# Kernel tuning notes

Hardware: AMD Instinct MI355X
Metric: run time of the kernel (lower is better)

## Reference

```python
import jax, jax.numpy as jnp
import numpy as np

N_LEVELS = 16
N_FEAT = 2
LOG2_T = 19
T = 2 ** LOG2_T
BASE_RES = 2 ** 4
MAX_RES = 2 ** 11
PER_LEVEL_SCALE = np.exp((np.log(MAX_RES) - np.log(BASE_RES)) / (N_LEVELS - 1))
RESOLUTIONS = [int(np.floor(BASE_RES * PER_LEVEL_SCALE ** lv)) + 1 for lv in range(N_LEVELS)]
INIT_ACTIVE_LEVEL = 8
N_POINTS = 1048576
N_OUT = N_LEVELS * N_FEAT
# tcnn spatial hashing primes
P1 = jnp.uint32(2654435761)
P2 = jnp.uint32(805459861)


def _level_lookup(x, tbl, res):
    """x: [N,3] in [0,1], tbl: [T,F], res: python int grid resolution."""
    pos = x * (res - 1)                       # [N,3]
    c0 = jnp.clip(jnp.floor(pos).astype(jnp.int32), 0, res - 2)
    w = pos - c0.astype(pos.dtype)            # [N,3] trilinear fractions
    feats = jnp.zeros((x.shape[0], tbl.shape[-1]), dtype=tbl.dtype)
    dense = (res ** 3) <= T                   # static per level: dense grid vs hashed
    for dz in (0, 1):
        for dy in (0, 1):
            for dx in (0, 1):
                offs = jnp.array([dx, dy, dz], jnp.int32)
                c = c0 + offs                 # [N,3] corner int coords
                if dense:
                    idx = c[:, 0] + res * (c[:, 1] + res * c[:, 2])
                else:
                    cu = c.astype(jnp.uint32)
                    idx = ((cu[:, 0]) ^ (cu[:, 1] * P1) ^ (cu[:, 2] * P2)) & jnp.uint32(T - 1)
                    idx = idx.astype(jnp.int32)
                # trilinear corner weight: prod over axes of (w if offs==1 else 1-w)
                wc = jnp.prod(jnp.where(offs == 1, w, 1.0 - w), axis=-1)  # [N]
                feats = feats + tbl[idx] * wc[:, None]
    return feats


def setup_inputs() -> dict:
    key = jax.random.key(0)
    k1, k2 = jax.random.split(key)
    x = jax.random.uniform(k1, (N_POINTS, 3), dtype=jnp.float32)
    # tcnn-style small uniform init of the hash table
    table = jax.random.uniform(k2, (N_LEVELS, T, N_FEAT), dtype=jnp.float32,
                               minval=-1e-4, maxval=1e-4)
    mask = jnp.concatenate([
        jnp.ones(INIT_ACTIVE_LEVEL * N_FEAT, jnp.float32),
        jnp.zeros((N_LEVELS - INIT_ACTIVE_LEVEL) * N_FEAT, jnp.float32),
    ])
    return {"x": x, "table": table, "mask": mask}


def reference(x, table, mask):
    # multi-resolution hash grid encoding + progressive level mask
    outs = [_level_lookup(x, table[lv], RESOLUTIONS[lv]) for lv in range(N_LEVELS)]
    enc = jnp.concatenate(outs, axis=-1)      # [N, 32]
    return enc * mask
```

## Files before the change

### kernel.cpp

```cpp
#include <hip/hip_runtime.h>
#include <cstdint>
#include <cstddef>


namespace {

constexpr int      kNLevels = 16;
constexpr uint32_t kT       = 1u << 19;
constexpr uint32_t kP1      = 2654435761u;
constexpr uint32_t kP2      = 805459861u;

typedef float v2f __attribute__((ext_vector_type(2)));
typedef float v4f __attribute__((ext_vector_type(4)));

__device__ constexpr int kRes[kNLevels] = {
    17, 23, 31, 43, 59, 81, 112, 154, 213, 295, 407, 562, 777, 1073, 1483, 2049
};

__device__ inline void corner_setup(float px, float py, float pz, int res,
                                    int& cx, int& cy, int& cz,
                                    float& wx, float& wy, float& wz) {
    const float s = (float)(res - 1);
    const float fx = px * s, fy = py * s, fz = pz * s;
    cx = (int)floorf(fx); cy = (int)floorf(fy); cz = (int)floorf(fz);
    cx = min(max(cx, 0), res - 2);
    cy = min(max(cy, 0), res - 2);
    cz = min(max(cz, 0), res - 2);
    wx = fx - (float)cx; wy = fy - (float)cy; wz = fz - (float)cz;
}

__global__ __launch_bounds__(256) void hashed_level_kernel(
    const float* __restrict__ x, const float* __restrict__ table,
    const float* __restrict__ mask, float* __restrict__ ws, int n)
{
    const int lv = 5 + blockIdx.y;
    const float m0 = mask[2 * lv], m1 = mask[2 * lv + 1];
    if (m0 == 0.0f && m1 == 0.0f) return;

    const int p = blockIdx.x * blockDim.x + threadIdx.x;
    if (p >= n) return;
    const float px = x[3 * p + 0];
    const float py = x[3 * p + 1];
    const float pz = x[3 * p + 2];

    const int res = kRes[lv];
    int cx, cy, cz; float wx, wy, wz;
    corner_setup(px, py, pz, res, cx, cy, cz, wx, wy, wz);
    const float ux = 1.0f - wx, uy = 1.0f - wy, uz = 1.0f - wz;
    const float* __restrict__ tbl = table + (size_t)lv * (size_t)(kT * 2);

    const uint32_t hy0 = (uint32_t)cy * kP1, hy1 = (uint32_t)(cy + 1) * kP1;
    const uint32_t hz0 = (uint32_t)cz * kP2, hz1 = (uint32_t)(cz + 1) * kP2;
    const uint32_t cxu = (uint32_t)cx;

    float r0 = 0.0f, r1 = 0.0f;
    if ((cx & 1) == 0) {
#pragma unroll
        for (int c = 0; c < 4; ++c) {
            const uint32_t h = ((c & 1) ? hy1 : hy0) ^ ((c >> 1) ? hz1 : hz0);
            const uint32_t i0 = (cxu ^ h) & (kT - 1u);
            const v4f ab = *(const v4f*)(tbl + 2u * (i0 & ~1u));
            const float wyz = ((c & 1) ? wy : uy) * ((c >> 1) ? wz : uz);
            const float w0 = ux * wyz, w1 = wx * wyz;
            const bool sw = (i0 & 1u) != 0u;
            r0 = fmaf(sw ? ab.z : ab.x, w0, fmaf(sw ? ab.x : ab.z, w1, r0));
            r1 = fmaf(sw ? ab.w : ab.y, w0, fmaf(sw ? ab.y : ab.w, w1, r1));
        }
    } else {
#pragma unroll
        for (int c = 0; c < 8; ++c) {
            const int dx = c & 1, dy = (c >> 1) & 1, dz = (c >> 2) & 1;
            const uint32_t idx =
                ((cxu + (uint32_t)dx) ^ (dy ? hy1 : hy0) ^ (dz ? hz1 : hz0))
                & (kT - 1u);
            const v2f v = *(const v2f*)(tbl + 2u * idx);
            const float w = (dx ? wx : ux) * (dy ? wy : uy) * (dz ? wz : uz);
            r0 = fmaf(v.x, w, r0);
            r1 = fmaf(v.y, w, r1);
        }
    }
    v2f o; o.x = r0; o.y = r1;
    __builtin_nontemporal_store(
        o, (v2f*)(ws + ((size_t)(lv - 5) * n + p) * 2));
}

__global__ __launch_bounds__(256) void gather_out_kernel(
    const float* __restrict__ x, const float* __restrict__ table,
    const float* __restrict__ ws, const float* __restrict__ mask,
    float* __restrict__ out, int n)
{
    __shared__ float lds[128 * 32];

    const int tid = threadIdx.x;
    const int p   = blockIdx.x * 256 + tid;
    const int pc  = (p < n) ? p : (n - 1);

    const float px = x[3 * pc + 0];
    const float py = x[3 * pc + 1];
    const float pz = x[3 * pc + 2];

    v4f o[8];

#pragma unroll
    for (int lv = 0; lv < 5; ++lv) {
        const float m0 = mask[2 * lv], m1 = mask[2 * lv + 1];
        float r0 = 0.0f, r1 = 0.0f;
        if (m0 != 0.0f || m1 != 0.0f) {
            const int res = kRes[lv];
            int cx, cy, cz; float wx, wy, wz;
            corner_setup(px, py, pz, res, cx, cy, cz, wx, wy, wz);
            const float ux = 1.0f - wx, uy = 1.0f - wy, uz = 1.0f - wz;
            const float* __restrict__ tbl = table + (size_t)lv * (size_t)(kT * 2);
#pragma unroll
            for (int c = 0; c < 4; ++c) {
                const int dy = c & 1, dz = (c >> 1) & 1;
                const uint32_t idx0 =
                    (uint32_t)(cx + res * ((cy + dy) + res * (cz + dz)));
                v4f ab;
                __builtin_memcpy(&ab, tbl + 2u * idx0, sizeof(v4f));
                const float wyz = (dy ? wy : uy) * (dz ? wz : uz);
                const float w0 = ux * wyz, w1 = wx * wyz;
                r0 = fmaf(ab.x, w0, fmaf(ab.z, w1, r0));
                r1 = fmaf(ab.y, w0, fmaf(ab.w, w1, r1));
            }
            r0 *= m0; r1 *= m1;
        }
        if (lv & 1) { o[lv >> 1].z = r0; o[lv >> 1].w = r1; }
        else        { o[lv >> 1].x = r0; o[lv >> 1].y = r1; }
    }

#pragma unroll
    for (int lv = 5; lv < kNLevels; ++lv) {
        const float m0 = mask[2 * lv], m1 = mask[2 * lv + 1];
        float r0 = 0.0f, r1 = 0.0f;
        if (m0 != 0.0f || m1 != 0.0f) {
            const v2f v = __builtin_nontemporal_load(
                (const v2f*)(ws + ((size_t)(lv - 5) * n + pc) * 2));
            r0 = v.x * m0;
            r1 = v.y * m1;
        }
        if (lv & 1) { o[lv >> 1].z = r0; o[lv >> 1].w = r1; }
        else        { o[lv >> 1].x = r0; o[lv >> 1].y = r1; }
    }

    const int r    = tid & 127;
    const int half = tid >> 7;
#pragma unroll
    for (int h = 0; h < 2; ++h) {
        if (h) __syncthreads();
        if (half == h) {
#pragma unroll
            for (int c = 0; c < 8; ++c)
                *(v4f*)&lds[r * 32 + ((c ^ (r & 7)) << 2)] = o[c];
        }
        __syncthreads();
        const long long bp = (long long)blockIdx.x * 256 + h * 128;
        float* const obase = out + (size_t)bp * 32;
#pragma unroll
        for (int j = 0; j < 4; ++j) {
            const int m  = tid + 256 * j;
            const int pr = m >> 3, c = m & 7;
            if (bp + pr < n) {
                const v4f v = *(const v4f*)&lds[pr * 32 + ((c ^ (pr & 7)) << 2)];
                __builtin_nontemporal_store(v, (v4f*)obase + m);
            }
        }
    }
}

__global__ __launch_bounds__(256) void fused_kernel(
    const float* __restrict__ x, const float* __restrict__ table,
    const float* __restrict__ mask, float* __restrict__ out, int n)
{
    const int p = blockIdx.x * blockDim.x + threadIdx.x;
    if (p >= n) return;
    const float px = x[3 * p + 0], py = x[3 * p + 1], pz = x[3 * p + 2];
    v4f o[8];
#pragma unroll
    for (int lv = 0; lv < kNLevels; ++lv) {
        const float m0 = mask[2 * lv], m1 = mask[2 * lv + 1];
        float r0 = 0.0f, r1 = 0.0f;
        if (m0 != 0.0f || m1 != 0.0f) {
            const int res = kRes[lv];
            const bool dense = ((long long)res * res * res) <= (long long)kT;
            int cx, cy, cz; float wx, wy, wz;
            corner_setup(px, py, pz, res, cx, cy, cz, wx, wy, wz);
            const float ux = 1.0f - wx, uy = 1.0f - wy, uz = 1.0f - wz;
            const float* __restrict__ tbl = table + (size_t)lv * (size_t)(kT * 2);
#pragma unroll
            for (int c = 0; c < 8; ++c) {
                const int dx = c & 1, dy = (c >> 1) & 1, dz = (c >> 2) & 1;
                const int ix = cx + dx, iy = cy + dy, iz = cz + dz;
                uint32_t idx;
                if (dense) idx = (uint32_t)(ix + res * (iy + res * iz));
                else idx = (((uint32_t)ix) ^ ((uint32_t)iy * kP1)
                                           ^ ((uint32_t)iz * kP2)) & (kT - 1u);
                const v2f v = *(const v2f*)(tbl + 2u * idx);
                const float w = (dx ? wx : ux) * (dy ? wy : uy) * (dz ? wz : uz);
                r0 = fmaf(v.x, w, r0);
                r1 = fmaf(v.y, w, r1);
            }
            r0 *= m0; r1 *= m1;
        }
        if (lv & 1) { o[lv >> 1].z = r0; o[lv >> 1].w = r1; }
        else        { o[lv >> 1].x = r0; o[lv >> 1].y = r1; }
    }
    v4f* __restrict__ op = (v4f*)(out + (size_t)p * 32);
#pragma unroll
    for (int i = 0; i < 8; ++i) op[i] = o[i];
}

}

extern "C" void kernel_launch(void* const* d_in, const int* in_sizes, int n_in,
                              void* d_out, int out_size, void* d_ws, size_t ws_size,
                              hipStream_t stream) {
    const float* x     = (const float*)d_in[0];
    const float* table = (const float*)d_in[1];
    const float* mask  = (const float*)d_in[2];
    float*       out   = (float*)d_out;

    const int n = in_sizes[0] / 3;
    const int block = 256;
    const int gx = (n + block - 1) / block;

    const size_t ws_needed = (size_t)(kNLevels - 5) * (size_t)n * 2 * sizeof(float);
    if (ws_size >= ws_needed) {
        float* ws = (float*)d_ws;
        dim3 grid1(gx, kNLevels - 5);
        hashed_level_kernel<<<grid1, block, 0, stream>>>(x, table, mask, ws, n);
        gather_out_kernel<<<gx, block, 0, stream>>>(x, table, ws, mask, out, n);
    } else {
        fused_kernel<<<gx, block, 0, stream>>>(x, table, mask, out, n);
    }
}
```

Baseline: 326.0 us.

## Simplify hashed gather, load workspace first, single-pass 32KB LDS transpose

```diff
diff --git a/kernel.cpp b/kernel.cpp
--- a/kernel.cpp
+++ b/kernel.cpp
@@ -29,6 +29,13 @@
     wx = fx - (float)cx; wy = fy - (float)cy; wz = fz - (float)cz;
 }
 
+__device__ inline void load_xyz(const float* __restrict__ x, int p,
+                                float& px, float& py, float& pz) {
+    float v[3];
+    __builtin_memcpy(v, x + 3 * (size_t)p, 12);
+    px = v[0]; py = v[1]; pz = v[2];
+}
+
 __global__ __launch_bounds__(256) void hashed_level_kernel(
     const float* __restrict__ x, const float* __restrict__ table,
     const float* __restrict__ mask, float* __restrict__ ws, int n)
@@ -39,9 +46,8 @@
 
     const int p = blockIdx.x * blockDim.x + threadIdx.x;
     if (p >= n) return;
-    const float px = x[3 * p + 0];
-    const float py = x[3 * p + 1];
-    const float pz = x[3 * p + 2];
+    float px, py, pz;
+    load_xyz(x, p, px, py, pz);
 
     const int res = kRes[lv];
     int cx, cy, cz; float wx, wy, wz;
@@ -54,30 +60,16 @@
     const uint32_t cxu = (uint32_t)cx;
 
     float r0 = 0.0f, r1 = 0.0f;
-    if ((cx & 1) == 0) {
-#pragma unroll
-        for (int c = 0; c < 4; ++c) {
-            const uint32_t h = ((c & 1) ? hy1 : hy0) ^ ((c >> 1) ? hz1 : hz0);
-            const uint32_t i0 = (cxu ^ h) & (kT - 1u);
-            const v4f ab = *(const v4f*)(tbl + 2u * (i0 & ~1u));
-            const float wyz = ((c & 1) ? wy : uy) * ((c >> 1) ? wz : uz);
-            const float w0 = ux * wyz, w1 = wx * wyz;
-            const bool sw = (i0 & 1u) != 0u;
-            r0 = fmaf(sw ? ab.z : ab.x, w0, fmaf(sw ? ab.x : ab.z, w1, r0));
-            r1 = fmaf(sw ? ab.w : ab.y, w0, fmaf(sw ? ab.y : ab.w, w1, r1));
-        }
-    } else {
-#pragma unroll
-        for (int c = 0; c < 8; ++c) {
-            const int dx = c & 1, dy = (c >> 1) & 1, dz = (c >> 2) & 1;
-            const uint32_t idx =
-                ((cxu + (uint32_t)dx) ^ (dy ? hy1 : hy0) ^ (dz ? hz1 : hz0))
-                & (kT - 1u);
-            const v2f v = *(const v2f*)(tbl + 2u * idx);
-            const float w = (dx ? wx : ux) * (dy ? wy : uy) * (dz ? wz : uz);
-            r0 = fmaf(v.x, w, r0);
-            r1 = fmaf(v.y, w, r1);
-        }
+#pragma unroll
+    for (int c = 0; c < 8; ++c) {
+        const int dx = c & 1, dy = (c >> 1) & 1, dz = (c >> 2) & 1;
+        const uint32_t idx =
+            ((cxu + (uint32_t)dx) ^ (dy ? hy1 : hy0) ^ (dz ? hz1 : hz0))
+            & (kT - 1u);
+        const v2f v = *(const v2f*)(tbl + 2u * idx);
+        const float w = (dx ? wx : ux) * (dy ? wy : uy) * (dz ? wz : uz);
+        r0 = fmaf(v.x, w, r0);
+        r1 = fmaf(v.y, w, r1);
     }
     v2f o; o.x = r0; o.y = r1;
     __builtin_nontemporal_store(
@@ -89,17 +81,30 @@
     const float* __restrict__ ws, const float* __restrict__ mask,
     float* __restrict__ out, int n)
 {
-    __shared__ float lds[128 * 32];
+    __shared__ float lds[256 * 32];
 
     const int tid = threadIdx.x;
     const int p   = blockIdx.x * 256 + tid;
     const int pc  = (p < n) ? p : (n - 1);
 
-    const float px = x[3 * pc + 0];
-    const float py = x[3 * pc + 1];
-    const float pz = x[3 * pc + 2];
+    float px, py, pz;
+    load_xyz(x, pc, px, py, pz);
 
     v4f o[8];
+
+#pragma unroll
+    for (int lv = 5; lv < kNLevels; ++lv) {
+        const float m0 = mask[2 * lv], m1 = mask[2 * lv + 1];
+        float r0 = 0.0f, r1 = 0.0f;
+        if (m0 != 0.0f || m1 != 0.0f) {
+            const v2f v = __builtin_nontemporal_load(
+                (const v2f*)(ws + ((size_t)(lv - 5) * n + pc) * 2));
+            r0 = v.x * m0;
+            r1 = v.y * m1;
+        }
+        if (lv & 1) { o[lv >> 1].z = r0; o[lv >> 1].w = r1; }
+        else        { o[lv >> 1].x = r0; o[lv >> 1].y = r1; }
+    }
 
 #pragma unroll
     for (int lv = 0; lv < 5; ++lv) {
@@ -130,40 +135,19 @@
     }
 
 #pragma unroll
-    for (int lv = 5; lv < kNLevels; ++lv) {
-        const float m0 = mask[2 * lv], m1 = mask[2 * lv + 1];
-        float r0 = 0.0f, r1 = 0.0f;
-        if (m0 != 0.0f || m1 != 0.0f) {
-            const v2f v = __builtin_nontemporal_load(
-                (const v2f*)(ws + ((size_t)(lv - 5) * n + pc) * 2));
-            r0 = v.x * m0;
-            r1 = v.y * m1;
-        }
-        if (lv & 1) { o[lv >> 1].z = r0; o[lv >> 1].w = r1; }
-        else        { o[lv >> 1].x = r0; o[lv >> 1].y = r1; }
-    }
-
-    const int r    = tid & 127;
-    const int half = tid >> 7;
-#pragma unroll
-    for (int h = 0; h < 2; ++h) {
-        if (h) __syncthreads();
-        if (half == h) {
-#pragma unroll
-            for (int c = 0; c < 8; ++c)
-                *(v4f*)&lds[r * 32 + ((c ^ (r & 7)) << 2)] = o[c];
-        }
-        __syncthreads();
-        const long long bp = (long long)blockIdx.x * 256 + h * 128;
-        float* const obase = out + (size_t)bp * 32;
-#pragma unroll
-        for (int j = 0; j < 4; ++j) {
-            const int m  = tid + 256 * j;
-            const int pr = m >> 3, c = m & 7;
-            if (bp + pr < n) {
-                const v4f v = *(const v4f*)&lds[pr * 32 + ((c ^ (pr & 7)) << 2)];
-                __builtin_nontemporal_store(v, (v4f*)obase + m);
-            }
+    for (int c = 0; c < 8; ++c)
+        *(v4f*)&lds[tid * 32 + ((c ^ (tid & 7)) << 2)] = o[c];
+    __syncthreads();
+
+    const long long bp = (long long)blockIdx.x * 256;
+    float* const obase = out + (size_t)bp * 32;
+#pragma unroll
+    for (int j = 0; j < 8; ++j) {
+        const int m  = tid + 256 * j;
+        const int pr = m >> 3, c = m & 7;
+        if (bp + pr < n) {
+            const v4f v = *(const v4f*)&lds[pr * 32 + ((c ^ (pr & 7)) << 2)];
+            __builtin_nontemporal_store(v, (v4f*)obase + m);
         }
     }
 }
```

Measured after the change: 325.1 us. Within noise of the previous version (-0.3%).
